# Optimization experiments

Measured on AMD Instinct MI355X. Metric: run time of the kernel, lower is better.

## Reference

```python
import jax, jax.numpy as jnp
import numpy as np

N_HEAD = 16

def setup_inputs() -> dict:
    key = jax.random.key(0)
    ks = jax.random.split(key, 5)
    B, T, C = 2, 2048, 1024
    s = 1.0 / np.sqrt(C)
    return {
        "x": jax.random.normal(ks[0], (B, T, C), dtype=jnp.float32),
        "Wq": jax.random.normal(ks[1], (C, C), dtype=jnp.float32) * s,
        "Wk": jax.random.normal(ks[2], (C, C), dtype=jnp.float32) * s,
        "Wv": jax.random.normal(ks[3], (C, C), dtype=jnp.float32) * s,
        "Wo": jax.random.normal(ks[4], (C, C), dtype=jnp.float32) * s,
        "bo": jnp.zeros((C,), dtype=jnp.float32),
    }

def reference(x, Wq, Wk, Wv, Wo, bo):
    B, T, C = x.shape
    H = N_HEAD
    D = C // H

    def shape(t):  # (B,T,C) -> (B,H,T,D)
        return t.reshape(B, T, H, D).transpose(0, 2, 1, 3)

    q = shape(x @ Wq)
    k = shape(x @ Wk)
    v = shape(x @ Wv)

    # scores: (B,H,T,Tk), Tk == T (no past_kv)
    att = jnp.einsum("bhtd,bhsd->bhts", q, k) * (1.0 / np.sqrt(D))
    i = jnp.arange(T)[:, None]
    j = jnp.arange(T)[None, :]
    causal = (j <= i)  # (T, Tk)
    att = jnp.where(causal[None, None], att, -jnp.inf)
    att = jax.nn.softmax(att, axis=-1)  # dropout=0.0 -> identity

    out = jnp.einsum("bhts,bhsd->bhtd", att, v)
    out = out.transpose(0, 2, 1, 3).reshape(B, T, C)
    out = out @ Wo + bo
    return out, (k, v)
```

## Files before the change

### kernel.cpp

```cpp
#include <hip/hip_runtime.h>
#include <hip/hip_bf16.h>

constexpr int B_ = 2;
constexpr int T_ = 2048;
constexpr int C_ = 1024;
constexpr int H_ = 16;
constexpr int D_ = 64;
constexpr int M_ = B_ * T_;

typedef __attribute__((ext_vector_type(8))) short bf16x8;
typedef __attribute__((ext_vector_type(4))) float f32x4;
typedef const __attribute__((address_space(1))) void gaddr_t;
typedef __attribute__((address_space(3))) void laddr_t;

__device__ __forceinline__ unsigned short f2bf(float f) {
    unsigned u = __float_as_uint(f);
    return (unsigned short)((u + 0x7fffu + ((u >> 16) & 1u)) >> 16);
}

union BF8 { bf16x8 v; __hip_bfloat162 h[4]; };

__device__ __forceinline__ bf16x8 cvt8(const float4 a, const float4 b) {
    BF8 r;
    r.h[0] = __float22bfloat162_rn(make_float2(a.x, a.y));
    r.h[1] = __float22bfloat162_rn(make_float2(a.z, a.w));
    r.h[2] = __float22bfloat162_rn(make_float2(b.x, b.y));
    r.h[3] = __float22bfloat162_rn(make_float2(b.z, b.w));
    return r.v;
}

__global__ __launch_bounds__(256)
void cast_x(const float* __restrict__ x, unsigned short* __restrict__ xb, int n4)
{
    for (int i = blockIdx.x * 256 + threadIdx.x; i < n4; i += gridDim.x * 256) {
        float4 v = ((const float4*)x)[i];
        union { __hip_bfloat162 h[2]; ushort4 u; } o;
        o.h[0] = __float22bfloat162_rn(make_float2(v.x, v.y));
        o.h[1] = __float22bfloat162_rn(make_float2(v.z, v.w));
        ((ushort4*)xb)[i] = o.u;
    }
}

__global__ __launch_bounds__(256)
void tcast_w(const float* __restrict__ Wq, const float* __restrict__ Wk,
             const float* __restrict__ Wv, const float* __restrict__ Wo,
             unsigned short* __restrict__ wtb)
{
    __shared__ float tile[64][65];
    const int z = blockIdx.z;
    const float* W = (z == 0) ? Wq : (z == 1) ? Wk : (z == 2) ? Wv : Wo;
    unsigned short* O = wtb + (size_t)z * C_ * C_;

    const int tid = threadIdx.x;
    const int n0 = blockIdx.x * 64, k0 = blockIdx.y * 64;
    const int r = tid >> 4, c4 = (tid & 15) * 4;

#pragma unroll
    for (int i = 0; i < 4; ++i) {
        const int kk = i * 16 + r;
        float4 v = *(const float4*)(W + (size_t)(k0 + kk) * C_ + n0 + c4);
        tile[c4 + 0][kk] = v.x;
        tile[c4 + 1][kk] = v.y;
        tile[c4 + 2][kk] = v.z;
        tile[c4 + 3][kk] = v.w;
    }
    __syncthreads();
#pragma unroll
    for (int i = 0; i < 4; ++i) {
        const int nn = i * 16 + r;
        ushort4 o;
        o.x = f2bf(tile[nn][c4 + 0]);
        o.y = f2bf(tile[nn][c4 + 1]);
        o.z = f2bf(tile[nn][c4 + 2]);
        o.w = f2bf(tile[nn][c4 + 3]);
        *(ushort4*)(O + (size_t)(n0 + nn) * C_ + k0 + c4) = o;
    }
}

template<int WRITE_KB>
__global__ __launch_bounds__(256)
void gemm_qkv(const unsigned short* __restrict__ xb, const unsigned short* __restrict__ wtb,
              unsigned short* __restrict__ qb, float* __restrict__ kout,
              float* __restrict__ vout, unsigned short* __restrict__ kb)
{
    __shared__ unsigned short As[128 * 64];
    __shared__ unsigned short Bs[128 * 64];

    const int tid = threadIdx.x;
    const int which = blockIdx.x >> 3;
    const int n0 = (blockIdx.x & 7) * 128;
    const int m0 = blockIdx.y * 128;
    const unsigned short* wt = wtb + (size_t)which * C_ * C_;

    const int lane = tid & 63, w = tid >> 6;
    const int wm = (w >> 1) * 64, wn = (w & 1) * 64;
    const int fr = lane & 15, qd = lane >> 4;

    f32x4 acc[4][4] = {};

    for (int k0 = 0; k0 < C_; k0 += 64) {
#pragma unroll
        for (int cc = 0; cc < 4; ++cc) {
            const int c = tid + cc * 256;
            const int row = c >> 3, dg = (c & 7) ^ (row & 7);
            __builtin_amdgcn_global_load_lds(
                (gaddr_t*)(xb + (size_t)(m0 + row) * C_ + k0 + dg * 8),
                (laddr_t*)((char*)As + (size_t)c * 16), 16, 0, 0);
        }
#pragma unroll
        for (int cc = 0; cc < 4; ++cc) {
            const int c = tid + cc * 256;
            const int row = c >> 3, dg = (c & 7) ^ (row & 7);
            __builtin_amdgcn_global_load_lds(
                (gaddr_t*)(wt + (size_t)(n0 + row) * C_ + k0 + dg * 8),
                (laddr_t*)((char*)Bs + (size_t)c * 16), 16, 0, 0);
        }
        __syncthreads();

#pragma unroll
        for (int half = 0; half < 2; ++half) {
            bf16x8 af[4], bfv[4];
#pragma unroll
            for (int mt = 0; mt < 4; ++mt) {
                const int row = wm + mt * 16 + fr, dg = half * 4 + qd;
                af[mt] = *(const bf16x8*)&As[row * 64 + ((dg ^ (row & 7)) * 8)];
            }
#pragma unroll
            for (int nt = 0; nt < 4; ++nt) {
                const int row = wn + nt * 16 + fr, dg = half * 4 + qd;
                bfv[nt] = *(const bf16x8*)&Bs[row * 64 + ((dg ^ (row & 7)) * 8)];
            }
#pragma unroll
            for (int mt = 0; mt < 4; ++mt)
#pragma unroll
                for (int nt = 0; nt < 4; ++nt)
                    acc[mt][nt] = __builtin_amdgcn_mfma_f32_16x16x32_bf16(
                        af[mt], bfv[nt], acc[mt][nt], 0, 0, 0);
        }
        __syncthreads();
    }

#pragma unroll
    for (int mt = 0; mt < 4; ++mt) {
#pragma unroll
        for (int nt = 0; nt < 4; ++nt) {
            const int ncol = n0 + wn + nt * 16 + fr;
            const int h = ncol >> 6, d = ncol & 63;
#pragma unroll
            for (int r = 0; r < 4; ++r) {
                const int mm = m0 + wm + mt * 16 + qd * 4 + r;
                const int b = mm >> 11, t = mm & (T_ - 1);
                const int bh = b * H_ + h;
                const size_t off = ((size_t)bh * T_ + t) * D_ + d;
                const float val = acc[mt][nt][r];
                if (which == 0)      qb[off]   = f2bf(val);
                else if (which == 1) {
                    kout[off] = val;
                    if (WRITE_KB) kb[off] = f2bf(val);
                } else               vout[off] = val;
            }
        }
    }
}

__global__ __launch_bounds__(256)
void transpose_v(const float* __restrict__ v, unsigned short* __restrict__ vtt)
{
    __shared__ unsigned short tile[64 * 66];
    const int tid = threadIdx.x;
    const int bh = blockIdx.y, t0 = blockIdx.x * 64;
    const float* vB = v + ((size_t)bh * T_ + t0) * D_;

    const int r = tid >> 4, c4 = (tid & 15) * 4;
#pragma unroll
    for (int i = 0; i < 4; ++i) {
        const int tt = i * 16 + r;
        float4 x4 = *(const float4*)(vB + tt * D_ + c4);
        tile[(c4 + 0) * 66 + tt] = f2bf(x4.x);
        tile[(c4 + 1) * 66 + tt] = f2bf(x4.y);
        tile[(c4 + 2) * 66 + tt] = f2bf(x4.z);
        tile[(c4 + 3) * 66 + tt] = f2bf(x4.w);
    }
    __syncthreads();
    unsigned short* out = vtt + (((size_t)bh * (T_ / 64) + (t0 >> 6)) * 64) * 64;
#pragma unroll
    for (int i = 0; i < 4; ++i) {
        const int d = i * 16 + r;
        ushort4 o;
        o.x = tile[d * 66 + c4 + 0];
        o.y = tile[d * 66 + c4 + 1];
        o.z = tile[d * 66 + c4 + 2];
        o.w = tile[d * 66 + c4 + 3];
        *(ushort4*)(out + d * 64 + c4) = o;
    }
}

__global__ __launch_bounds__(256)
void gemm_o(const unsigned short* __restrict__ ab, const unsigned short* __restrict__ wot,
            const float* __restrict__ bo, float* __restrict__ out)
{
    __shared__ unsigned short As[128 * 64];
    __shared__ unsigned short Bs[128 * 64];

    const int tid = threadIdx.x;
    const int n0 = blockIdx.x * 128;
    const int m0 = blockIdx.y * 128;

    const int lane = tid & 63, w = tid >> 6;
    const int wm = (w >> 1) * 64, wn = (w & 1) * 64;
    const int fr = lane & 15, qd = lane >> 4;

    f32x4 acc[4][4] = {};

    for (int k0 = 0; k0 < C_; k0 += 64) {
#pragma unroll
        for (int cc = 0; cc < 4; ++cc) {
            const int c = tid + cc * 256;
            const int row = c >> 3, dg = (c & 7) ^ (row & 7);
            __builtin_amdgcn_global_load_lds(
                (gaddr_t*)(ab + (size_t)(m0 + row) * C_ + k0 + dg * 8),
                (laddr_t*)((char*)As + (size_t)c * 16), 16, 0, 0);
        }
#pragma unroll
        for (int cc = 0; cc < 4; ++cc) {
            const int c = tid + cc * 256;
            const int row = c >> 3, dg = (c & 7) ^ (row & 7);
            __builtin_amdgcn_global_load_lds(
                (gaddr_t*)(wot + (size_t)(n0 + row) * C_ + k0 + dg * 8),
                (laddr_t*)((char*)Bs + (size_t)c * 16), 16, 0, 0);
        }
        __syncthreads();

#pragma unroll
        for (int half = 0; half < 2; ++half) {
            bf16x8 af[4], bfv[4];
#pragma unroll
            for (int mt = 0; mt < 4; ++mt) {
                const int row = wm + mt * 16 + fr, dg = half * 4 + qd;
                af[mt] = *(const bf16x8*)&As[row * 64 + ((dg ^ (row & 7)) * 8)];
            }
#pragma unroll
            for (int nt = 0; nt < 4; ++nt) {
                const int row = wn + nt * 16 + fr, dg = half * 4 + qd;
                bfv[nt] = *(const bf16x8*)&Bs[row * 64 + ((dg ^ (row & 7)) * 8)];
            }
#pragma unroll
            for (int mt = 0; mt < 4; ++mt)
#pragma unroll
                for (int nt = 0; nt < 4; ++nt)
                    acc[mt][nt] = __builtin_amdgcn_mfma_f32_16x16x32_bf16(
                        af[mt], bfv[nt], acc[mt][nt], 0, 0, 0);
        }
        __syncthreads();
    }

#pragma unroll
    for (int mt = 0; mt < 4; ++mt) {
#pragma unroll
        for (int nt = 0; nt < 4; ++nt) {
            const int ncol = n0 + wn + nt * 16 + fr;
            const float bb = bo[ncol];
#pragma unroll
            for (int r = 0; r < 4; ++r) {
                const int mm = m0 + wm + mt * 16 + qd * 4 + r;
                out[(size_t)mm * C_ + ncol] = acc[mt][nt][r] + bb;
            }
        }
    }
}

__global__ __launch_bounds__(256)
void attn_lds(const unsigned short* __restrict__ qb, const unsigned short* __restrict__ kb,
              const unsigned short* __restrict__ vtt, unsigned short* __restrict__ attb)
{
    __shared__ unsigned short Ks[64 * 64];
    __shared__ unsigned short Vs[64 * 64];
    __shared__ alignas(16) unsigned short Pt[4][16 * 72];

    const int tid = threadIdx.x;
    const int lane = tid & 63, w = tid >> 6;
    const int fr = lane & 15, qd = lane >> 4;

    const int blk = blockIdx.x;
    const int xcd = blk & 7, within = blk >> 3;
    const int bh = xcd * 4 + (within & 3);
    const int jj = within >> 2;
    const int kk_ = jj >> 3, ii_ = jj & 7;
    const int qt = (kk_ == 0) ? (31 - ii_) : (kk_ == 1) ? ii_
                 : (kk_ == 2) ? (23 - ii_) : (8 + ii_);
    const int b = bh >> 4, h = bh & 15;

    unsigned short* Pw = Pt[w];
    const unsigned short* qB = qb  + (size_t)bh * T_ * D_;
    const unsigned short* kB = kb  + (size_t)bh * T_ * D_;
    const unsigned short* vT = vtt + (size_t)bh * (T_ / 64) * 64 * 64;

    const int qr0 = qt * 64 + w * 16;
    const int qrow_g = qr0 + fr;

    bf16x8 aq0 = *(const bf16x8*)(qB + (size_t)(qr0 + fr) * D_ + qd * 8);
    bf16x8 aq1 = *(const bf16x8*)(qB + (size_t)(qr0 + fr) * D_ + 32 + qd * 8);

    f32x4 accT[4] = {};
    float l_i = 0.0f;
    const float sc2 = 0.18033688f;

    const int L0 = w * 128 + lane, L1 = L0 + 64;
    const int r0 = L0 >> 3, e0 = (((L0 & 7) ^ (r0 & 7)) * 8);
    const int r1 = L1 >> 3, e1 = (((L1 & 7) ^ (r1 & 7)) * 8);
    laddr_t* dK0 = (laddr_t*)((char*)Ks + (size_t)L0 * 16);
    laddr_t* dK1 = (laddr_t*)((char*)Ks + (size_t)L1 * 16);
    laddr_t* dV0 = (laddr_t*)((char*)Vs + (size_t)L0 * 16);
    laddr_t* dV1 = (laddr_t*)((char*)Vs + (size_t)L1 * 16);

    for (int jt = 0; jt <= qt; ++jt) {
        __syncthreads();
        {
            const unsigned short* kt = kB + (size_t)(jt * 64) * 64;
            const unsigned short* vt = vT + (size_t)jt * 4096;
            __builtin_amdgcn_global_load_lds((gaddr_t*)(kt + r0 * 64 + e0), dK0, 16, 0, 0);
            __builtin_amdgcn_global_load_lds((gaddr_t*)(kt + r1 * 64 + e1), dK1, 16, 0, 0);
            __builtin_amdgcn_global_load_lds((gaddr_t*)(vt + r0 * 64 + e0), dV0, 16, 0, 0);
            __builtin_amdgcn_global_load_lds((gaddr_t*)(vt + r1 * 64 + e1), dV1, 16, 0, 0);
        }
        __syncthreads();

        bf16x8 bk[8];
#pragma unroll
        for (int q8 = 0; q8 < 8; ++q8) {
            const int row = (q8 >> 1) * 16 + fr;
            const int dg = (q8 & 1) * 4 + qd;
            bk[q8] = *(const bf16x8*)&Ks[row * 64 + ((dg ^ (row & 7)) * 8)];
        }

        f32x4 s4[4] = {};
#pragma unroll
        for (int nt = 0; nt < 4; ++nt) {
            s4[nt] = __builtin_amdgcn_mfma_f32_16x16x32_bf16(bk[nt * 2 + 0], aq0, s4[nt], 0, 0, 0);
            s4[nt] = __builtin_amdgcn_mfma_f32_16x16x32_bf16(bk[nt * 2 + 1], aq1, s4[nt], 0, 0, 0);
        }

        if (jt == qt) {
            const int kbase = jt * 64 + qd * 4;
#pragma unroll
            for (int nt = 0; nt < 4; ++nt)
#pragma unroll
            for (int r = 0; r < 4; ++r) {
                const int kcol = kbase + nt * 16 + r;
                const float pv = (kcol <= qrow_g)
                               ? __builtin_amdgcn_exp2f(s4[nt][r] * sc2) : 0.0f;
                s4[nt][r] = pv;
                l_i += pv;
            }
        } else {
#pragma unroll
            for (int nt = 0; nt < 4; ++nt)
#pragma unroll
            for (int r = 0; r < 4; ++r) {
                const float pv = __builtin_amdgcn_exp2f(s4[nt][r] * sc2);
                s4[nt][r] = pv;
                l_i += pv;
            }
        }

#pragma unroll
        for (int nt = 0; nt < 4; ++nt) {
            union { __hip_bfloat162 h2[2]; unsigned long long u; } pk;
            pk.h2[0] = __float22bfloat162_rn(make_float2(s4[nt][0], s4[nt][1]));
            pk.h2[1] = __float22bfloat162_rn(make_float2(s4[nt][2], s4[nt][3]));
            *(unsigned long long*)&Pw[fr * 72 + nt * 16 + qd * 4] = pk.u;
        }
        const bf16x8 ap0 = *(const bf16x8*)&Pw[fr * 72 + qd * 8];
        const bf16x8 ap1 = *(const bf16x8*)&Pw[fr * 72 + 32 + qd * 8];

        bf16x8 bv[8];
#pragma unroll
        for (int q8 = 0; q8 < 8; ++q8) {
            const int row = (q8 >> 1) * 16 + fr;
            const int dg = (q8 & 1) * 4 + qd;
            bv[q8] = *(const bf16x8*)&Vs[row * 64 + ((dg ^ (row & 7)) * 8)];
        }

#pragma unroll
        for (int nt = 0; nt < 4; ++nt) {
            accT[nt] = __builtin_amdgcn_mfma_f32_16x16x32_bf16(bv[nt * 2 + 0], ap0, accT[nt], 0, 0, 0);
            accT[nt] = __builtin_amdgcn_mfma_f32_16x16x32_bf16(bv[nt * 2 + 1], ap1, accT[nt], 0, 0, 0);
        }
    }

    l_i += __shfl_xor(l_i, 16);
    l_i += __shfl_xor(l_i, 32);
    const float inv = 1.0f / l_i;

#pragma unroll
    for (int nt = 0; nt < 4; ++nt) {
        union { __hip_bfloat162 h2[2]; unsigned long long u; } ok;
        ok.h2[0] = __float22bfloat162_rn(make_float2(accT[nt][0] * inv, accT[nt][1] * inv));
        ok.h2[1] = __float22bfloat162_rn(make_float2(accT[nt][2] * inv, accT[nt][3] * inv));
        *(unsigned long long*)&Pw[fr * 72 + nt * 16 + qd * 4] = ok.u;
    }
    {
        const int row = lane >> 2, d0 = (lane & 3) * 16;
        const bf16x8 o0 = *(const bf16x8*)&Pw[row * 72 + d0];
        const bf16x8 o1 = *(const bf16x8*)&Pw[row * 72 + d0 + 8];
        unsigned short* op = attb + ((size_t)b * T_ + qr0 + row) * C_ + h * 64 + d0;
        *(bf16x8*)op = o0;
        *(bf16x8*)(op + 8) = o1;
    }
}

__global__ __launch_bounds__(256)
void attn_v4(const unsigned short* __restrict__ qb, const float* __restrict__ kf,
             const unsigned short* __restrict__ vtt, unsigned short* __restrict__ attb)
{
    __shared__ alignas(16) unsigned short Pt[4][16 * 72];

    const int tid = threadIdx.x;
    const int lane = tid & 63, w = tid >> 6;
    const int fr = lane & 15, qd = lane >> 4;

    const int blk = blockIdx.x;
    const int xcd = blk & 7, within = blk >> 3;
    const int bh = xcd * 4 + (within & 3);
    const int jj = within >> 2;
    const int kk_ = jj >> 3, ii_ = jj & 7;
    const int qt = (kk_ == 0) ? (31 - ii_) : (kk_ == 1) ? ii_
                 : (kk_ == 2) ? (23 - ii_) : (8 + ii_);
    const int b = bh >> 4, h = bh & 15;

    unsigned short* Pw = Pt[w];
    const unsigned short* qB = qb  + (size_t)bh * T_ * D_;
    const float*          kB = kf  + (size_t)bh * T_ * D_;
    const unsigned short* vT = vtt + (size_t)bh * (T_ / 64) * 64 * 64;

    const int qr0 = qt * 64 + w * 16;
    const int qrow_g = qr0 + fr;

    bf16x8 aq0 = *(const bf16x8*)(qB + (size_t)(qr0 + fr) * D_ + qd * 8);
    bf16x8 aq1 = *(const bf16x8*)(qB + (size_t)(qr0 + fr) * D_ + 32 + qd * 8);

    f32x4 accT[4] = {};
    float l_i = 0.0f;
    const float sc2 = 0.18033688f;

    for (int jt = 0; jt <= qt; ++jt) {
        bf16x8 bk[8];
#pragma unroll
        for (int q8 = 0; q8 < 8; ++q8) {
            const float* p = kB + (size_t)(jt * 64 + (q8 >> 1) * 16 + fr) * D_
                           + (q8 & 1) * 32 + qd * 8;
            bk[q8] = cvt8(*(const float4*)p, *(const float4*)(p + 4));
        }
        f32x4 s4[4] = {};
#pragma unroll
        for (int nt = 0; nt < 4; ++nt) {
            s4[nt] = __builtin_amdgcn_mfma_f32_16x16x32_bf16(bk[nt * 2 + 0], aq0, s4[nt], 0, 0, 0);
            s4[nt] = __builtin_amdgcn_mfma_f32_16x16x32_bf16(bk[nt * 2 + 1], aq1, s4[nt], 0, 0, 0);
        }
        if (jt == qt) {
            const int kbase = jt * 64 + qd * 4;
#pragma unroll
            for (int nt = 0; nt < 4; ++nt)
#pragma unroll
            for (int r = 0; r < 4; ++r) {
                const int kcol = kbase + nt * 16 + r;
                const float pv = (kcol <= qrow_g)
                               ? __builtin_amdgcn_exp2f(s4[nt][r] * sc2) : 0.0f;
                s4[nt][r] = pv; l_i += pv;
            }
        } else {
#pragma unroll
            for (int nt = 0; nt < 4; ++nt)
#pragma unroll
            for (int r = 0; r < 4; ++r) {
                const float pv = __builtin_amdgcn_exp2f(s4[nt][r] * sc2);
                s4[nt][r] = pv; l_i += pv;
            }
        }
#pragma unroll
        for (int nt = 0; nt < 4; ++nt) {
            union { __hip_bfloat162 h2[2]; unsigned long long u; } pk;
            pk.h2[0] = __float22bfloat162_rn(make_float2(s4[nt][0], s4[nt][1]));
            pk.h2[1] = __float22bfloat162_rn(make_float2(s4[nt][2], s4[nt][3]));
            *(unsigned long long*)&Pw[fr * 72 + nt * 16 + qd * 4] = pk.u;
        }
        const bf16x8 ap0 = *(const bf16x8*)&Pw[fr * 72 + qd * 8];
        const bf16x8 ap1 = *(const bf16x8*)&Pw[fr * 72 + 32 + qd * 8];

        bf16x8 bv[8];
#pragma unroll
        for (int q8 = 0; q8 < 8; ++q8)
            bv[q8] = *(const bf16x8*)(vT + (size_t)jt * 4096
                                      + ((q8 >> 1) * 16 + fr) * 64 + (q8 & 1) * 32 + qd * 8);
#pragma unroll
        for (int nt = 0; nt < 4; ++nt) {
            accT[nt] = __builtin_amdgcn_mfma_f32_16x16x32_bf16(bv[nt * 2 + 0], ap0, accT[nt], 0, 0, 0);
            accT[nt] = __builtin_amdgcn_mfma_f32_16x16x32_bf16(bv[nt * 2 + 1], ap1, accT[nt], 0, 0, 0);
        }
    }

    l_i += __shfl_xor(l_i, 16);
    l_i += __shfl_xor(l_i, 32);
    const float inv = 1.0f / l_i;
#pragma unroll
    for (int nt = 0; nt < 4; ++nt) {
        union { __hip_bfloat162 h2[2]; unsigned long long u; } ok;
        ok.h2[0] = __float22bfloat162_rn(make_float2(accT[nt][0] * inv, accT[nt][1] * inv));
        ok.h2[1] = __float22bfloat162_rn(make_float2(accT[nt][2] * inv, accT[nt][3] * inv));
        *(unsigned long long*)&Pw[fr * 72 + nt * 16 + qd * 4] = ok.u;
    }
    {
        const int row = lane >> 2, d0 = (lane & 3) * 16;
        const bf16x8 o0 = *(const bf16x8*)&Pw[row * 72 + d0];
        const bf16x8 o1 = *(const bf16x8*)&Pw[row * 72 + d0 + 8];
        unsigned short* op = attb + ((size_t)b * T_ + qr0 + row) * C_ + h * 64 + d0;
        *(bf16x8*)op = o0;
        *(bf16x8*)(op + 8) = o1;
    }
}

extern "C" void kernel_launch(void* const* d_in, const int* in_sizes, int n_in,
                              void* d_out, int out_size, void* d_ws, size_t ws_size,
                              hipStream_t stream)
{
    (void)in_sizes; (void)n_in; (void)out_size;
    const float* x  = (const float*)d_in[0];
    const float* Wq = (const float*)d_in[1];
    const float* Wk = (const float*)d_in[2];
    const float* Wv = (const float*)d_in[3];
    const float* Wo = (const float*)d_in[4];
    const float* bo = (const float*)d_in[5];

    float* out  = (float*)d_out;
    float* kout = out  + (size_t)M_ * C_;
    float* vout = kout + (size_t)B_ * H_ * T_ * D_;

    unsigned short* xb   = (unsigned short*)d_ws;
    unsigned short* wtb  = xb  + (size_t)M_ * C_;
    unsigned short* qb   = wtb + (size_t)4 * C_ * C_;
    unsigned short* vtt  = qb  + (size_t)M_ * C_;
    unsigned short* kb   = vtt + (size_t)M_ * C_;
    unsigned short* attb = xb;
    const bool use_kb = ws_size >= (size_t)40 * 1024 * 1024;

    cast_x<<<1024, 256, 0, stream>>>(x, xb, (M_ * C_) / 4);
    tcast_w<<<dim3(16, 16, 4), 256, 0, stream>>>(Wq, Wk, Wv, Wo, wtb);

    if (use_kb)
        gemm_qkv<1><<<dim3(24, M_ / 128), 256, 0, stream>>>(xb, wtb, qb, kout, vout, kb);
    else
        gemm_qkv<0><<<dim3(24, M_ / 128), 256, 0, stream>>>(xb, wtb, qb, kout, vout, kb);

    transpose_v<<<dim3(T_ / 64, B_ * H_), 256, 0, stream>>>(vout, vtt);

    if (use_kb)
        attn_lds<<<1024, 256, 0, stream>>>(qb, kb, vtt, attb);
    else
        attn_v4<<<1024, 256, 0, stream>>>(qb, kout, vtt, attb);

    gemm_o<<<dim3(8, M_ / 128), 256, 0, stream>>>(attb, wtb + (size_t)3 * C_ * C_, bo, out);
}
```

Measured before the change: 202.3 us.

## Double-buffer LDS tiles in QKV, output-projection and attention kernels

Adds a second shared-memory buffer to the two GEMM kernels and the attention kernel. The async global-to-LDS load for the next K tile (or K/V block) is issued right after the barrier, so it runs while MFMA compute uses the current buffer. This drops one barrier per iteration and is meant to hide global load latency behind compute. The cost is double the LDS per block in the GEMMs (64KB), which can lower how many blocks fit on each CU.

Result: slower. 217.1 us (+7.3%).

```diff
diff --git a/kernel.cpp b/kernel.cpp
--- a/kernel.cpp
+++ b/kernel.cpp
@@ -83,8 +83,8 @@
               unsigned short* __restrict__ qb, float* __restrict__ kout,
               float* __restrict__ vout, unsigned short* __restrict__ kb)
 {
-    __shared__ unsigned short As[128 * 64];
-    __shared__ unsigned short Bs[128 * 64];
+    __shared__ unsigned short As[2][128 * 64];
+    __shared__ unsigned short Bs[2][128 * 64];
 
     const int tid = threadIdx.x;
     const int which = blockIdx.x >> 3;
@@ -96,16 +96,14 @@
     const int wm = (w >> 1) * 64, wn = (w & 1) * 64;
     const int fr = lane & 15, qd = lane >> 4;
 
-    f32x4 acc[4][4] = {};
-
-    for (int k0 = 0; k0 < C_; k0 += 64) {
+    auto dma = [&](int k0, int buf) {
 #pragma unroll
         for (int cc = 0; cc < 4; ++cc) {
             const int c = tid + cc * 256;
             const int row = c >> 3, dg = (c & 7) ^ (row & 7);
             __builtin_amdgcn_global_load_lds(
                 (gaddr_t*)(xb + (size_t)(m0 + row) * C_ + k0 + dg * 8),
-                (laddr_t*)((char*)As + (size_t)c * 16), 16, 0, 0);
+                (laddr_t*)((char*)As[buf] + (size_t)c * 16), 16, 0, 0);
         }
 #pragma unroll
         for (int cc = 0; cc < 4; ++cc) {
@@ -113,9 +111,18 @@
             const int row = c >> 3, dg = (c & 7) ^ (row & 7);
             __builtin_amdgcn_global_load_lds(
                 (gaddr_t*)(wt + (size_t)(n0 + row) * C_ + k0 + dg * 8),
-                (laddr_t*)((char*)Bs + (size_t)c * 16), 16, 0, 0);
-        }
+                (laddr_t*)((char*)Bs[buf] + (size_t)c * 16), 16, 0, 0);
+        }
+    };
+
+    f32x4 acc[4][4] = {};
+
+    dma(0, 0);
+    for (int ki = 0; ki < 16; ++ki) {
         __syncthreads();
+        if (ki < 15) dma((ki + 1) * 64, (ki + 1) & 1);
+        const unsigned short* Ab = As[ki & 1];
+        const unsigned short* Bb = Bs[ki & 1];
 
 #pragma unroll
         for (int half = 0; half < 2; ++half) {
@@ -123,12 +130,12 @@
 #pragma unroll
             for (int mt = 0; mt < 4; ++mt) {
                 const int row = wm + mt * 16 + fr, dg = half * 4 + qd;
-                af[mt] = *(const bf16x8*)&As[row * 64 + ((dg ^ (row & 7)) * 8)];
+                af[mt] = *(const bf16x8*)&Ab[row * 64 + ((dg ^ (row & 7)) * 8)];
             }
 #pragma unroll
             for (int nt = 0; nt < 4; ++nt) {
                 const int row = wn + nt * 16 + fr, dg = half * 4 + qd;
-                bfv[nt] = *(const bf16x8*)&Bs[row * 64 + ((dg ^ (row & 7)) * 8)];
+                bfv[nt] = *(const bf16x8*)&Bb[row * 64 + ((dg ^ (row & 7)) * 8)];
             }
 #pragma unroll
             for (int mt = 0; mt < 4; ++mt)
@@ -137,7 +144,6 @@
                     acc[mt][nt] = __builtin_amdgcn_mfma_f32_16x16x32_bf16(
                         af[mt], bfv[nt], acc[mt][nt], 0, 0, 0);
         }
-        __syncthreads();
     }
 
 #pragma unroll
@@ -199,8 +205,8 @@
 void gemm_o(const unsigned short* __restrict__ ab, const unsigned short* __restrict__ wot,
             const float* __restrict__ bo, float* __restrict__ out)
 {
-    __shared__ unsigned short As[128 * 64];
-    __shared__ unsigned short Bs[128 * 64];
+    __shared__ unsigned short As[2][128 * 64];
+    __shared__ unsigned short Bs[2][128 * 64];
 
     const int tid = threadIdx.x;
     const int n0 = blockIdx.x * 128;
@@ -210,16 +216,14 @@
     const int wm = (w >> 1) * 64, wn = (w & 1) * 64;
     const int fr = lane & 15, qd = lane >> 4;
 
-    f32x4 acc[4][4] = {};
-
-    for (int k0 = 0; k0 < C_; k0 += 64) {
+    auto dma = [&](int k0, int buf) {
 #pragma unroll
         for (int cc = 0; cc < 4; ++cc) {
             const int c = tid + cc * 256;
             const int row = c >> 3, dg = (c & 7) ^ (row & 7);
             __builtin_amdgcn_global_load_lds(
                 (gaddr_t*)(ab + (size_t)(m0 + row) * C_ + k0 + dg * 8),
-                (laddr_t*)((char*)As + (size_t)c * 16), 16, 0, 0);
+                (laddr_t*)((char*)As[buf] + (size_t)c * 16), 16, 0, 0);
         }
 #pragma unroll
         for (int cc = 0; cc < 4; ++cc) {
@@ -227,9 +231,18 @@
             const int row = c >> 3, dg = (c & 7) ^ (row & 7);
             __builtin_amdgcn_global_load_lds(
                 (gaddr_t*)(wot + (size_t)(n0 + row) * C_ + k0 + dg * 8),
-                (laddr_t*)((char*)Bs + (size_t)c * 16), 16, 0, 0);
-        }
+                (laddr_t*)((char*)Bs[buf] + (size_t)c * 16), 16, 0, 0);
+        }
+    };
+
+    f32x4 acc[4][4] = {};
+
+    dma(0, 0);
+    for (int ki = 0; ki < 16; ++ki) {
         __syncthreads();
+        if (ki < 15) dma((ki + 1) * 64, (ki + 1) & 1);
+        const unsigned short* Ab = As[ki & 1];
+        const unsigned short* Bb = Bs[ki & 1];
 
 #pragma unroll
         for (int half = 0; half < 2; ++half) {
@@ -237,12 +250,12 @@
 #pragma unroll
             for (int mt = 0; mt < 4; ++mt) {
                 const int row = wm + mt * 16 + fr, dg = half * 4 + qd;
-                af[mt] = *(const bf16x8*)&As[row * 64 + ((dg ^ (row & 7)) * 8)];
+                af[mt] = *(const bf16x8*)&Ab[row * 64 + ((dg ^ (row & 7)) * 8)];
             }
 #pragma unroll
             for (int nt = 0; nt < 4; ++nt) {
                 const int row = wn + nt * 16 + fr, dg = half * 4 + qd;
-                bfv[nt] = *(const bf16x8*)&Bs[row * 64 + ((dg ^ (row & 7)) * 8)];
+                bfv[nt] = *(const bf16x8*)&Bb[row * 64 + ((dg ^ (row & 7)) * 8)];
             }
 #pragma unroll
             for (int mt = 0; mt < 4; ++mt)
@@ -251,7 +264,6 @@
                     acc[mt][nt] = __builtin_amdgcn_mfma_f32_16x16x32_bf16(
                         af[mt], bfv[nt], acc[mt][nt], 0, 0, 0);
         }
-        __syncthreads();
     }
 
 #pragma unroll
@@ -273,8 +285,8 @@
 void attn_lds(const unsigned short* __restrict__ qb, const unsigned short* __restrict__ kb,
               const unsigned short* __restrict__ vtt, unsigned short* __restrict__ attb)
 {
-    __shared__ unsigned short Ks[64 * 64];
-    __shared__ unsigned short Vs[64 * 64];
+    __shared__ unsigned short Ks[2][64 * 64];
+    __shared__ unsigned short Vs[2][64 * 64];
     __shared__ alignas(16) unsigned short Pt[4][16 * 72];
 
     const int tid = threadIdx.x;
@@ -308,29 +320,33 @@
     const int L0 = w * 128 + lane, L1 = L0 + 64;
     const int r0 = L0 >> 3, e0 = (((L0 & 7) ^ (r0 & 7)) * 8);
     const int r1 = L1 >> 3, e1 = (((L1 & 7) ^ (r1 & 7)) * 8);
-    laddr_t* dK0 = (laddr_t*)((char*)Ks + (size_t)L0 * 16);
-    laddr_t* dK1 = (laddr_t*)((char*)Ks + (size_t)L1 * 16);
-    laddr_t* dV0 = (laddr_t*)((char*)Vs + (size_t)L0 * 16);
-    laddr_t* dV1 = (laddr_t*)((char*)Vs + (size_t)L1 * 16);
-
+
+    auto dmaKV = [&](int j, int buf) {
+        const unsigned short* kt = kB + (size_t)(j * 64) * 64;
+        const unsigned short* vt = vT + (size_t)j * 4096;
+        __builtin_amdgcn_global_load_lds((gaddr_t*)(kt + r0 * 64 + e0),
+            (laddr_t*)((char*)Ks[buf] + (size_t)L0 * 16), 16, 0, 0);
+        __builtin_amdgcn_global_load_lds((gaddr_t*)(kt + r1 * 64 + e1),
+            (laddr_t*)((char*)Ks[buf] + (size_t)L1 * 16), 16, 0, 0);
+        __builtin_amdgcn_global_load_lds((gaddr_t*)(vt + r0 * 64 + e0),
+            (laddr_t*)((char*)Vs[buf] + (size_t)L0 * 16), 16, 0, 0);
+        __builtin_amdgcn_global_load_lds((gaddr_t*)(vt + r1 * 64 + e1),
+            (laddr_t*)((char*)Vs[buf] + (size_t)L1 * 16), 16, 0, 0);
+    };
+
+    dmaKV(0, 0);
     for (int jt = 0; jt <= qt; ++jt) {
         __syncthreads();
-        {
-            const unsigned short* kt = kB + (size_t)(jt * 64) * 64;
-            const unsigned short* vt = vT + (size_t)jt * 4096;
-            __builtin_amdgcn_global_load_lds((gaddr_t*)(kt + r0 * 64 + e0), dK0, 16, 0, 0);
-            __builtin_amdgcn_global_load_lds((gaddr_t*)(kt + r1 * 64 + e1), dK1, 16, 0, 0);
-            __builtin_amdgcn_global_load_lds((gaddr_t*)(vt + r0 * 64 + e0), dV0, 16, 0, 0);
-            __builtin_amdgcn_global_load_lds((gaddr_t*)(vt + r1 * 64 + e1), dV1, 16, 0, 0);
-        }
-        __syncthreads();
+        if (jt < qt) dmaKV(jt + 1, (jt + 1) & 1);
+        const unsigned short* Kb = Ks[jt & 1];
+        const unsigned short* Vb = Vs[jt & 1];
 
         bf16x8 bk[8];
 #pragma unroll
         for (int q8 = 0; q8 < 8; ++q8) {
             const int row = (q8 >> 1) * 16 + fr;
             const int dg = (q8 & 1) * 4 + qd;
-            bk[q8] = *(const bf16x8*)&Ks[row * 64 + ((dg ^ (row & 7)) * 8)];
+            bk[q8] = *(const bf16x8*)&Kb[row * 64 + ((dg ^ (row & 7)) * 8)];
         }
 
         f32x4 s4[4] = {};
@@ -378,7 +394,7 @@
         for (int q8 = 0; q8 < 8; ++q8) {
             const int row = (q8 >> 1) * 16 + fr;
             const int dg = (q8 & 1) * 4 + qd;
-            bv[q8] = *(const bf16x8*)&Vs[row * 64 + ((dg ^ (row & 7)) * 8)];
+            bv[q8] = *(const bf16x8*)&Vb[row * 64 + ((dg ^ (row & 7)) * 8)];
         }
 
 #pragma unroll
```
